# Performance work log

Measured on AMD Instinct MI355X. Metric: run time of the kernel, lower is better.

The kernel has to match this reference:

```python
import jax, jax.numpy as jnp
import numpy as np

P = 2          # patch size
DEPTH = 3
NHEAD = 8
DROP_RATIO = 0.15
LN_EPS = 1e-5


def _ln(x, g, b):
    m = jnp.mean(x, axis=-1, keepdims=True)
    v = jnp.mean((x - m) ** 2, axis=-1, keepdims=True)
    return (x - m) * jax.lax.rsqrt(v + LN_EPS) * g + b


def setup_inputs() -> dict:
    key = jax.random.key(0)
    ks = jax.random.split(key, 16)
    B, C, HW, D, L = 4, 3, 96, 256, DEPTH
    N = (HW // P) ** 2
    s = 0.02
    return {
        "x": jax.random.normal(ks[0], (B, C, HW, HW), jnp.float32),
        "patch_w": jax.random.normal(ks[1], (D, C, P, P), jnp.float32) * s,
        "patch_b": jnp.zeros((D,), jnp.float32),
        "pos": jax.random.normal(ks[2], (1, N, D), jnp.float32) * s,
        "imp_w1": jax.random.normal(ks[3], (D, 256), jnp.float32) * s,
        "imp_b1": jnp.zeros((256,), jnp.float32),
        "imp_w2": jax.random.normal(ks[4], (256, 1), jnp.float32) * s,
        "imp_b2": jnp.zeros((1,), jnp.float32),
        "ln1_g": jnp.ones((L, D), jnp.float32),
        "ln1_b": jnp.zeros((L, D), jnp.float32),
        "qkv_w": jax.random.normal(ks[5], (L, D, 3 * D), jnp.float32) * s,
        "qkv_b": jnp.zeros((L, 3 * D), jnp.float32),
        "proj_w": jax.random.normal(ks[6], (L, D, D), jnp.float32) * s,
        "proj_b": jnp.zeros((L, D), jnp.float32),
        "ln2_g": jnp.ones((L, D), jnp.float32),
        "ln2_b": jnp.zeros((L, D), jnp.float32),
        "mlp_w1": jax.random.normal(ks[7], (L, D, 4 * D), jnp.float32) * s,
        "mlp_b1": jnp.zeros((L, 4 * D), jnp.float32),
        "mlp_w2": jax.random.normal(ks[8], (L, 4 * D, D), jnp.float32) * s,
        "mlp_b2": jnp.zeros((L, D), jnp.float32),
        "out_g": jnp.ones((D,), jnp.float32),
        "out_b": jnp.zeros((D,), jnp.float32),
    }


def reference(x, patch_w, patch_b, pos, imp_w1, imp_b1, imp_w2, imp_b2,
              ln1_g, ln1_b, qkv_w, qkv_b, proj_w, proj_b,
              ln2_g, ln2_b, mlp_w1, mlp_b1, mlp_w2, mlp_b2, out_g, out_b):
    B, C, H, W = x.shape
    D = patch_w.shape[0]
    Hc, Wc = H // P, W // P
    # Patch embed: conv(k=stride=P) == blocked einsum  -> (B, N, D)
    xr = x.reshape(B, C, Hc, P, Wc, P)
    tokens = jnp.einsum('bchpwq,dcpq->bhwd', xr, patch_w).reshape(B, Hc * Wc, D) + patch_b
    tokens = tokens + pos
    B, N, _ = tokens.shape

    # Importance scores -> bottom-k keys masked (Eq.8-10)
    h = jax.nn.relu(tokens @ imp_w1 + imp_b1)
    scores = jax.nn.sigmoid((h @ imp_w2 + imp_b2)[..., 0])  # (B, N)
    k = int(DROP_RATIO * N)
    _, idx = jax.lax.top_k(-scores, k)                      # k smallest scores
    md = jnp.zeros((B, N), bool).at[jnp.arange(B)[:, None], idx].set(True)

    dk = D // NHEAD
    scale = 1.0 / np.sqrt(dk)
    for l in range(DEPTH):
        hln = _ln(tokens, ln1_g[l], ln1_b[l])
        qkv = hln @ qkv_w[l] + qkv_b[l]
        q, kk, v = jnp.split(qkv, 3, axis=-1)
        q = q.reshape(B, N, NHEAD, dk).transpose(0, 2, 1, 3)
        kk = kk.reshape(B, N, NHEAD, dk).transpose(0, 2, 1, 3)
        v = v.reshape(B, N, NHEAD, dk).transpose(0, 2, 1, 3)
        logits = jnp.einsum('bhnd,bhmd->bhnm', q, kk) * scale
        logits = jnp.where(md[:, None, None, :], -jnp.inf, logits)
        attn = jax.nn.softmax(logits, axis=-1)
        out = jnp.einsum('bhnm,bhmd->bhnd', attn, v)
        out = out.transpose(0, 2, 1, 3).reshape(B, N, D)
        tokens = tokens + (out @ proj_w[l] + proj_b[l])
        h2 = _ln(tokens, ln2_g[l], ln2_b[l])
        tokens = tokens + (jax.nn.gelu(h2 @ mlp_w1[l] + mlp_b1[l], approximate=False) @ mlp_w2[l] + mlp_b2[l])

    tokens = _ln(tokens, out_g, out_b)
    return tokens.mean(axis=1)  # (B, D)
```

## Files before the change

kernel.cpp:

```cpp
#include <hip/hip_runtime.h>
#include <hip/hip_bf16.h>
#include <math.h>

#define BATCH 4
#define NTOK  2304
#define DIM   256
#define NHEADS 8
#define HCDIM 48
#define KSEL  345
#define NKEEP 1959
#define NKC   1984
#define KT    31
#define KREM  39
#define LN_EPS 1e-5f
#define QSCALE 0.25508688726880056f

typedef unsigned short u16;
typedef __attribute__((ext_vector_type(8))) short bf16x8;
typedef __attribute__((ext_vector_type(4))) float f32x4;

__device__ __forceinline__ u16 f2bf(float x) {
  union { float f; unsigned u; } v; v.f = x;
  return (u16)((v.u + 0x7FFFu + ((v.u >> 16) & 1u)) >> 16);
}

__device__ __forceinline__ void gload_lds16(const u16* g, u16* l) {
  __builtin_amdgcn_global_load_lds((const __attribute__((address_space(1))) void*)g,
                                   (__attribute__((address_space(3))) void*)l, 16, 0, 0);
}

__global__ __launch_bounds__(256) void k_patch_embed(
    const float* __restrict__ x, const float* __restrict__ pw,
    const float* __restrict__ pb, const float* __restrict__ pos,
    float* __restrict__ tokens) {
  int blk = blockIdx.x;
  int b = blk / NTOK, n = blk % NTOK;
  int hc = n / HCDIM, wc = n % HCDIM;
  __shared__ float xs[12];
  int t = threadIdx.x;
  if (t < 12) {
    int c = t >> 2, p = (t >> 1) & 1, q = t & 1;
    xs[t] = x[((b * 3 + c) * 96 + (hc * 2 + p)) * 96 + (wc * 2 + q)];
  }
  __syncthreads();
  float acc = pb[t];
#pragma unroll
  for (int i = 0; i < 12; ++i) acc += xs[i] * pw[t * 12 + i];
  tokens[(size_t)(b * NTOK + n) * DIM + t] = acc + pos[n * DIM + t];
}

__global__ __launch_bounds__(256) void k_importance(
    const float* __restrict__ tokens, const float* __restrict__ w1,
    const float* __restrict__ b1, const float* __restrict__ w2,
    const float* __restrict__ b2, float* __restrict__ scores) {
  __shared__ float ts[16 * 256];
  __shared__ float hw[16 * 256];
  int base = blockIdx.x * 16;
  int t = threadIdx.x;
  for (int i = t; i < 16 * 256; i += 256) ts[i] = tokens[(size_t)base * 256 + i];
  __syncthreads();
  float acc[16];
#pragma unroll
  for (int r = 0; r < 16; ++r) acc[r] = b1[t];
  for (int i = 0; i < 256; ++i) {
    float w = w1[i * 256 + t];
#pragma unroll
    for (int r = 0; r < 16; ++r) acc[r] += ts[r * 256 + i] * w;
  }
  float w2v = w2[t];
#pragma unroll
  for (int r = 0; r < 16; ++r) hw[r * 256 + t] = fmaxf(acc[r], 0.f) * w2v;
  __syncthreads();
  if (t < 16) {
    float s = b2[0];
    for (int i = 0; i < 256; ++i) s += hw[t * 256 + i];
    scores[base + t] = 1.f / (1.f + expf(-s));
  }
}

__global__ __launch_bounds__(256) void k_select(const float* __restrict__ scores,
                                                int* __restrict__ cmap,
                                                u16* __restrict__ kvc) {
  int b = blockIdx.x, t = threadIdx.x;
  __shared__ unsigned sb[NTOK];
  __shared__ int cnt;
  __shared__ int pfl[256], pfe[256];
  __shared__ int remS;
  for (int i = t; i < NTOK; i += 256) sb[i] = __float_as_uint(scores[b * NTOK + i]);
  __syncthreads();
  unsigned prefix = 0;
  int r = KSEL;
  for (int bit = 31; bit >= 0; --bit) {
    if (t == 0) cnt = 0;
    __syncthreads();
    unsigned bmask = 1u << bit;
    unsigned hmask = (bit == 31) ? 0u : ~((bmask << 1) - 1u);
    int local = 0;
    for (int i = t; i < NTOK; i += 256)
      if ((sb[i] & hmask) == prefix && !(sb[i] & bmask)) local++;
    if (local) atomicAdd(&cnt, local);
    __syncthreads();
    int c0 = cnt;
    if (r > c0) { r -= c0; prefix |= bmask; }
    __syncthreads();
  }
  unsigned v = prefix;
  int cl = 0, ce = 0;
  int j0 = t * 9;
  for (int j = j0; j < j0 + 9; ++j) { cl += (sb[j] < v); ce += (sb[j] == v); }
  pfl[t] = cl; pfe[t] = ce;
  __syncthreads();
  if (t == 0) {
    int pl = 0, pe = 0;
    for (int i = 0; i < 256; ++i) {
      int a = pfl[i], e = pfe[i];
      pfl[i] = pl; pfe[i] = pe;
      pl += a; pe += e;
    }
    remS = KSEL - pl;
  }
  __syncthreads();
  int pl = pfl[t], pe = pfe[t], rem = remS;
  for (int j = j0; j < j0 + 9; ++j) {
    bool less = sb[j] < v, eq = sb[j] == v;
    bool drop = less || (eq && pe < rem);
    int dropped_before = pl + (pe < rem ? pe : rem);
    cmap[b * NTOK + j] = drop ? -1 : (j - dropped_before);
    pl += less; pe += eq;
  }
  for (int i = t; i < (NKC - NKEEP) * 512; i += 256)
    kvc[((size_t)b * NKC + NKEEP) * 512 + i] = 0;
}

__global__ __launch_bounds__(256) void k_ln4bf(
    const float* __restrict__ in, u16* __restrict__ out,
    const float* __restrict__ g, const float* __restrict__ bta) {
  int w = threadIdx.x >> 6, l = threadIdx.x & 63;
  size_t row = (size_t)blockIdx.x * 4 + w;
  float4 v = *(const float4*)(in + row * DIM + l * 4);
  float s = v.x + v.y + v.z + v.w;
  float ss = v.x * v.x + v.y * v.y + v.z * v.z + v.w * v.w;
#pragma unroll
  for (int o = 1; o < 64; o <<= 1) { s += __shfl_xor(s, o); ss += __shfl_xor(ss, o); }
  float m = s * (1.f / DIM);
  float inv = rsqrtf(ss * (1.f / DIM) - m * m + LN_EPS);
  float4 gv = *(const float4*)(g + l * 4);
  float4 bv = *(const float4*)(bta + l * 4);
  union { ushort4 u4; __hip_bfloat162 h2[2]; } o4;
  o4.h2[0] = __float22bfloat162_rn(make_float2((v.x - m) * inv * gv.x + bv.x,
                                               (v.y - m) * inv * gv.y + bv.y));
  o4.h2[1] = __float22bfloat162_rn(make_float2((v.z - m) * inv * gv.z + bv.z,
                                               (v.w - m) * inv * gv.w + bv.w));
  *(ushort4*)(out + row * DIM + l * 4) = o4.u4;
}

__global__ __launch_bounds__(256) void k_lnmean(
    const float* __restrict__ in, const float* __restrict__ g,
    const float* __restrict__ bta, float* __restrict__ part) {
  int chunk = blockIdx.x, b = blockIdx.y;
  int w = threadIdx.x >> 6, l = threadIdx.x & 63;
  float4 gv = *(const float4*)(g + l * 4);
  float4 bv = *(const float4*)(bta + l * 4);
  float4 acc = make_float4(0.f, 0.f, 0.f, 0.f);
  for (int i = 0; i < 16; ++i) {
    size_t row = (size_t)b * NTOK + chunk * 64 + w * 16 + i;
    float4 v = *(const float4*)(in + row * DIM + l * 4);
    float s = v.x + v.y + v.z + v.w;
    float ss = v.x * v.x + v.y * v.y + v.z * v.z + v.w * v.w;
#pragma unroll
    for (int o = 1; o < 64; o <<= 1) { s += __shfl_xor(s, o); ss += __shfl_xor(ss, o); }
    float m = s * (1.f / DIM);
    float inv = rsqrtf(ss * (1.f / DIM) - m * m + LN_EPS);
    acc.x += (v.x - m) * inv * gv.x + bv.x;
    acc.y += (v.y - m) * inv * gv.y + bv.y;
    acc.z += (v.z - m) * inv * gv.z + bv.z;
    acc.w += (v.w - m) * inv * gv.w + bv.w;
  }
  __shared__ float4 red[4][64];
  red[w][l] = acc;
  __syncthreads();
  if (w == 0) {
    float4 a0 = red[0][l], a1 = red[1][l], a2 = red[2][l], a3 = red[3][l];
    float4 tot = make_float4(a0.x + a1.x + a2.x + a3.x, a0.y + a1.y + a2.y + a3.y,
                             a0.z + a1.z + a2.z + a3.z, a0.w + a1.w + a2.w + a3.w);
    *(float4*)(part + ((size_t)b * 36 + chunk) * DIM + l * 4) = tot;
  }
}

__global__ __launch_bounds__(256) void k_mean_final(const float* __restrict__ part,
                                                    float* __restrict__ out) {
  int b = blockIdx.x, d = threadIdx.x;
  float s = 0.f;
  for (int c = 0; c < 36; ++c) s += part[(size_t)(b * 36 + c) * DIM + d];
  out[b * DIM + d] = s * (1.0f / NTOK);
}

__global__ __launch_bounds__(256) void k_wtrans_all(
    const float* __restrict__ qkv_w, const float* __restrict__ proj_w,
    const float* __restrict__ mlp_w1, const float* __restrict__ mlp_w2,
    u16* __restrict__ wq, u16* __restrict__ wp,
    u16* __restrict__ w1, u16* __restrict__ w2) {
  int id = blockIdx.x;
  const float* W; u16* WT; int K, N, m;
  if (id < 576)       { m = id;        K = 256;  N = 768;  W = qkv_w;  WT = wq; }
  else if (id < 768)  { m = id - 576;  K = 256;  N = 256;  W = proj_w; WT = wp; }
  else if (id < 1536) { m = id - 768;  K = 256;  N = 1024; W = mlp_w1; WT = w1; }
  else                { m = id - 1536; K = 1024; N = 256;  W = mlp_w2; WT = w2; }
  int ntiles = N / 32, tilesPerLayer = ntiles * (K / 32);
  int layer = m / tilesPerLayer, tid = m % tilesPerLayer;
  int nb = (tid % ntiles) * 32, kb = (tid / ntiles) * 32;
  const float* Wl = W + (size_t)layer * K * N;
  u16* WTl = WT + (size_t)layer * K * N;
  __shared__ float tile[32][33];
  int tx = threadIdx.x & 31, ty = threadIdx.x >> 5;
  for (int i = 0; i < 32; i += 8) tile[ty + i][tx] = Wl[(size_t)(kb + ty + i) * N + nb + tx];
  __syncthreads();
  for (int i = 0; i < 32; i += 8)
    WTl[(size_t)(nb + ty + i) * K + kb + tx] = f2bf(tile[tx][ty + i]);
}

__global__ __launch_bounds__(256) void k_gemm_bf16(
    const u16* __restrict__ A, const u16* __restrict__ BT,
    const float* __restrict__ bias, u16* __restrict__ outb,
    int K, int N, int act) {
  __shared__ __align__(16) u16 As[2][128 * 32];
  __shared__ __align__(16) u16 Bs[2][128 * 32];
  int t = threadIdx.x;
  int m0 = blockIdx.y * 128, n0 = blockIdx.x * 128;
  int w = t >> 6, l = t & 63, lr = l & 15, qd = l >> 4;
  int wm = (w >> 1) * 64, wn = (w & 1) * 64;
  int sc = ((t & 3) ^ ((t >> 4) & 3)) * 8;
  int rc = (qd ^ ((lr >> 2) & 3)) * 8;
  const u16* gA = A + (size_t)(m0 + w * 16 + (l >> 2)) * K + sc;
  const u16* gA2 = gA + (size_t)64 * K;
  const u16* gB = BT + (size_t)(n0 + w * 16 + (l >> 2)) * K + sc;
  const u16* gB2 = gB + (size_t)64 * K;
  f32x4 acc[4][4];
#pragma unroll
  for (int i = 0; i < 4; ++i)
#pragma unroll
    for (int j = 0; j < 4; ++j)
#pragma unroll
      for (int r = 0; r < 4; ++r) acc[i][j][r] = 0.f;
  gload_lds16(gA, As[0] + w * 512);
  gload_lds16(gA2, As[0] + 2048 + w * 512);
  gload_lds16(gB, Bs[0] + w * 512);
  gload_lds16(gB2, Bs[0] + 2048 + w * 512);
  int nchunks = K >> 5;
  for (int c = 0; c < nchunks; ++c) {
    int buf = c & 1;
    __syncthreads();
    if (c + 1 < nchunks) {
      int k0 = (c + 1) << 5;
      gload_lds16(gA + k0, As[buf ^ 1] + w * 512);
      gload_lds16(gA2 + k0, As[buf ^ 1] + 2048 + w * 512);
      gload_lds16(gB + k0, Bs[buf ^ 1] + w * 512);
      gload_lds16(gB2 + k0, Bs[buf ^ 1] + 2048 + w * 512);
    }
    bf16x8 af[4], bfr[4];
#pragma unroll
    for (int mt = 0; mt < 4; ++mt)
      af[mt] = *(const bf16x8*)(As[buf] + (wm + mt * 16 + lr) * 32 + rc);
#pragma unroll
    for (int nt = 0; nt < 4; ++nt)
      bfr[nt] = *(const bf16x8*)(Bs[buf] + (wn + nt * 16 + lr) * 32 + rc);
#pragma unroll
    for (int mt = 0; mt < 4; ++mt)
#pragma unroll
      for (int nt = 0; nt < 4; ++nt)
        acc[mt][nt] = __builtin_amdgcn_mfma_f32_16x16x32_bf16(af[mt], bfr[nt],
                                                              acc[mt][nt], 0, 0, 0);
  }
#pragma unroll
  for (int mt = 0; mt < 4; ++mt) {
#pragma unroll
    for (int nt = 0; nt < 4; ++nt) {
#pragma unroll
      for (int r = 0; r < 4; ++r) {
        size_t m = (size_t)m0 + wm + mt * 16 + qd * 4 + r;
        int c = n0 + wn + nt * 16 + lr;
        float val = acc[mt][nt][r] + bias[c];
        if (act) val = 0.5f * val * (1.f + erff(val * 0.70710678118654752f));
        outb[m * N + c] = f2bf(val);
      }
    }
  }
}

__global__ __launch_bounds__(256) void k_gemm_qkv(
    const u16* __restrict__ A, const u16* __restrict__ BT,
    const float* __restrict__ bias, const int* __restrict__ cmap,
    u16* __restrict__ Qb, u16* __restrict__ KVc) {
  const int K = 256, N = 768;
  __shared__ __align__(16) u16 As[2][128 * 32];
  __shared__ __align__(16) u16 Bs[2][128 * 32];
  int t = threadIdx.x;
  int m0 = blockIdx.y * 128, n0 = blockIdx.x * 128;
  int w = t >> 6, l = t & 63, lr = l & 15, qd = l >> 4;
  int wm = (w >> 1) * 64, wn = (w & 1) * 64;
  int sc = ((t & 3) ^ ((t >> 4) & 3)) * 8;
  int rc = (qd ^ ((lr >> 2) & 3)) * 8;
  const u16* gA = A + (size_t)(m0 + w * 16 + (l >> 2)) * K + sc;
  const u16* gA2 = gA + (size_t)64 * K;
  const u16* gB = BT + (size_t)(n0 + w * 16 + (l >> 2)) * K + sc;
  const u16* gB2 = gB + (size_t)64 * K;
  f32x4 acc[4][4];
#pragma unroll
  for (int i = 0; i < 4; ++i)
#pragma unroll
    for (int j = 0; j < 4; ++j)
#pragma unroll
      for (int r = 0; r < 4; ++r) acc[i][j][r] = 0.f;
  gload_lds16(gA, As[0] + w * 512);
  gload_lds16(gA2, As[0] + 2048 + w * 512);
  gload_lds16(gB, Bs[0] + w * 512);
  gload_lds16(gB2, Bs[0] + 2048 + w * 512);
  for (int c = 0; c < 8; ++c) {
    int buf = c & 1;
    __syncthreads();
    if (c + 1 < 8) {
      int k0 = (c + 1) << 5;
      gload_lds16(gA + k0, As[buf ^ 1] + w * 512);
      gload_lds16(gA2 + k0, As[buf ^ 1] + 2048 + w * 512);
      gload_lds16(gB + k0, Bs[buf ^ 1] + w * 512);
      gload_lds16(gB2 + k0, Bs[buf ^ 1] + 2048 + w * 512);
    }
    bf16x8 af[4], bfr[4];
#pragma unroll
    for (int mt = 0; mt < 4; ++mt)
      af[mt] = *(const bf16x8*)(As[buf] + (wm + mt * 16 + lr) * 32 + rc);
#pragma unroll
    for (int nt = 0; nt < 4; ++nt)
      bfr[nt] = *(const bf16x8*)(Bs[buf] + (wn + nt * 16 + lr) * 32 + rc);
#pragma unroll
    for (int mt = 0; mt < 4; ++mt)
#pragma unroll
      for (int nt = 0; nt < 4; ++nt)
        acc[mt][nt] = __builtin_amdgcn_mfma_f32_16x16x32_bf16(af[mt], bfr[nt],
                                                              acc[mt][nt], 0, 0, 0);
  }
  bool isQ = (n0 + wn) < 256;
#pragma unroll
  for (int mt = 0; mt < 4; ++mt) {
#pragma unroll
    for (int r = 0; r < 4; ++r) {
      int m = m0 + wm + mt * 16 + qd * 4 + r;
      int cpos = isQ ? 0 : cmap[m];
      int b = m / NTOK;
#pragma unroll
      for (int nt = 0; nt < 4; ++nt) {
        int c = n0 + wn + nt * 16 + lr;
        float val = acc[mt][nt][r] + bias[c];
        if (isQ) {
          Qb[(size_t)m * 256 + c] = f2bf(val * QSCALE);
        } else if (cpos >= 0) {
          KVc[((size_t)b * NKC + cpos) * 512 + (c - 256)] = f2bf(val);
        }
      }
    }
  }
}

__global__ __launch_bounds__(256) void k_gemm_n64(
    const u16* __restrict__ A, const u16* __restrict__ BT,
    const float* __restrict__ bias, const float* __restrict__ res,
    float* __restrict__ outf, int K, int N) {
  __shared__ __align__(16) u16 As[2][64 * 32];
  __shared__ __align__(16) u16 Bs[2][64 * 32];
  int t = threadIdx.x;
  int m0 = blockIdx.y * 64, n0 = blockIdx.x * 64;
  int w = t >> 6, l = t & 63, lr = l & 15, qd = l >> 4;
  int wm = (w >> 1) * 32, wn = (w & 1) * 32;
  int sc = ((t & 3) ^ ((t >> 4) & 3)) * 8;
  int rc = (qd ^ ((lr >> 2) & 3)) * 8;
  const u16* gA = A + (size_t)(m0 + w * 16 + (l >> 2)) * K + sc;
  const u16* gB = BT + (size_t)(n0 + w * 16 + (l >> 2)) * K + sc;
  f32x4 acc[2][2];
#pragma unroll
  for (int i = 0; i < 2; ++i)
#pragma unroll
    for (int j = 0; j < 2; ++j)
#pragma unroll
      for (int r = 0; r < 4; ++r) acc[i][j][r] = 0.f;
  gload_lds16(gA, As[0] + w * 512);
  gload_lds16(gB, Bs[0] + w * 512);
  int nchunks = K >> 5;
  for (int c = 0; c < nchunks; ++c) {
    int buf = c & 1;
    __syncthreads();
    if (c + 1 < nchunks) {
      int k0 = (c + 1) << 5;
      gload_lds16(gA + k0, As[buf ^ 1] + w * 512);
      gload_lds16(gB + k0, Bs[buf ^ 1] + w * 512);
    }
    bf16x8 af[2], bfr[2];
#pragma unroll
    for (int mt = 0; mt < 2; ++mt)
      af[mt] = *(const bf16x8*)(As[buf] + (wm + mt * 16 + lr) * 32 + rc);
#pragma unroll
    for (int nt = 0; nt < 2; ++nt)
      bfr[nt] = *(const bf16x8*)(Bs[buf] + (wn + nt * 16 + lr) * 32 + rc);
#pragma unroll
    for (int mt = 0; mt < 2; ++mt)
#pragma unroll
      for (int nt = 0; nt < 2; ++nt)
        acc[mt][nt] = __builtin_amdgcn_mfma_f32_16x16x32_bf16(af[mt], bfr[nt],
                                                              acc[mt][nt], 0, 0, 0);
  }
#pragma unroll
  for (int mt = 0; mt < 2; ++mt) {
#pragma unroll
    for (int nt = 0; nt < 2; ++nt) {
#pragma unroll
      for (int r = 0; r < 4; ++r) {
        size_t m = (size_t)m0 + wm + mt * 16 + qd * 4 + r;
        int c = n0 + wn + nt * 16 + lr;
        outf[m * N + c] = acc[mt][nt][r] + bias[c] + res[m * N + c];
      }
    }
  }
}

__global__ __launch_bounds__(256) void k_attn6(
    const u16* __restrict__ Qb, const u16* __restrict__ KVc,
    u16* __restrict__ outb) {
  int qt = blockIdx.x, h = blockIdx.y, b = blockIdx.z;
  int t = threadIdx.x, w = t >> 6, l = t & 63, lr = l & 15, qd = l >> 4;
  __shared__ __align__(16) u16 Ks[2][64 * 32];
  __shared__ __align__(16) u16 Vt[2][32][72];
  __shared__ __align__(16) u16 Pq[4][16][72];
  const short ONE = (short)0x3F80;
  int q0 = qt * 64 + w * 16;
  bf16x8 qf = *(const bf16x8*)(Qb + ((size_t)(b * NTOK) + q0 + lr) * 256 + h * 32 + qd * 8);
  const u16* kvb = KVc + (size_t)b * NKC * 512;
  const u16* gK = kvb + (size_t)(t >> 2) * 512 + h * 32 + ((t & 3) ^ ((t >> 4) & 3)) * 8;
  const u16* gV = kvb + (size_t)l * 512 + 256 + h * 32 + w * 8;
  int rc = (qd ^ ((lr >> 2) & 3)) * 8;
  gload_lds16(gK, &Ks[0][w * 512]);
  bf16x8 vr = *(const bf16x8*)(gV);
  f32x4 oa[2];
  f32x4 lacc;
#pragma unroll
  for (int r = 0; r < 4; ++r) { oa[0][r] = 0.f; oa[1][r] = 0.f; lacc[r] = 0.f; }
  bf16x8 ones;
#pragma unroll
  for (int j = 0; j < 8; ++j) ones[j] = ONE;
  for (int kt = 0; kt < KT; ++kt) {
    int buf = kt & 1;
#pragma unroll
    for (int j = 0; j < 8; ++j) Vt[buf][w * 8 + j][l] = (u16)vr[j];
    __syncthreads();
    if (kt + 1 < KT) {
      size_t off = (size_t)(kt + 1) * 64 * 512;
      gload_lds16(gK + off, &Ks[buf ^ 1][w * 512]);
      vr = *(const bf16x8*)(gV + off);
    }
    f32x4 p4[4];
#pragma unroll
    for (int nt = 0; nt < 4; ++nt) {
      bf16x8 kf = *(const bf16x8*)(&Ks[buf][(nt * 16 + lr) * 32 + rc]);
      f32x4 z; z[0] = 0.f; z[1] = 0.f; z[2] = 0.f; z[3] = 0.f;
      p4[nt] = __builtin_amdgcn_mfma_f32_16x16x32_bf16(kf, qf, z, 0, 0, 0);
    }
#pragma unroll
    for (int nt = 0; nt < 4; ++nt)
#pragma unroll
      for (int r = 0; r < 4; ++r) p4[nt][r] = __builtin_amdgcn_exp2f(p4[nt][r]);
#pragma unroll
    for (int nt = 0; nt < 4; ++nt) {
      union { ushort4 u4; __hip_bfloat162 h2[2]; } pu;
      pu.h2[0] = __float22bfloat162_rn(make_float2(p4[nt][0], p4[nt][1]));
      pu.h2[1] = __float22bfloat162_rn(make_float2(p4[nt][2], p4[nt][3]));
      *(ushort4*)(&Pq[w][lr][nt * 16 + qd * 4]) = pu.u4;
    }
    bf16x8 of1 = ones;
    if (kt == KT - 1) {
#pragma unroll
      for (int j = 0; j < 8; ++j) of1[j] = (32 + qd * 8 + j < KREM) ? ONE : (short)0;
    }
#pragma unroll
    for (int kh = 0; kh < 2; ++kh) {
      bf16x8 pf = *(const bf16x8*)(&Pq[w][lr][kh * 32 + qd * 8]);
#pragma unroll
      for (int dh = 0; dh < 2; ++dh) {
        bf16x8 vf = *(const bf16x8*)(&Vt[buf][dh * 16 + lr][kh * 32 + qd * 8]);
        oa[dh] = __builtin_amdgcn_mfma_f32_16x16x32_bf16(pf, vf, oa[dh], 0, 0, 0);
      }
      lacc = __builtin_amdgcn_mfma_f32_16x16x32_bf16(pf, kh ? of1 : ones, lacc, 0, 0, 0);
    }
  }
#pragma unroll
  for (int r = 0; r < 4; ++r) {
    float inv = 1.f / lacc[r];
    size_t row = (size_t)b * NTOK + q0 + qd * 4 + r;
    outb[row * 256 + h * 32 + lr] = f2bf(oa[0][r] * inv);
    outb[row * 256 + h * 32 + 16 + lr] = f2bf(oa[1][r] * inv);
  }
}

extern "C" void kernel_launch(void* const* d_in, const int* in_sizes, int n_in,
                              void* d_out, int out_size, void* d_ws, size_t ws_size,
                              hipStream_t stream) {
  (void)in_sizes; (void)n_in; (void)out_size;
  const float* x       = (const float*)d_in[0];
  const float* patch_w = (const float*)d_in[1];
  const float* patch_b = (const float*)d_in[2];
  const float* pos     = (const float*)d_in[3];
  const float* imp_w1  = (const float*)d_in[4];
  const float* imp_b1  = (const float*)d_in[5];
  const float* imp_w2  = (const float*)d_in[6];
  const float* imp_b2  = (const float*)d_in[7];
  const float* ln1_g   = (const float*)d_in[8];
  const float* ln1_b   = (const float*)d_in[9];
  const float* qkv_w   = (const float*)d_in[10];
  const float* qkv_b   = (const float*)d_in[11];
  const float* proj_w  = (const float*)d_in[12];
  const float* proj_b  = (const float*)d_in[13];
  const float* ln2_g   = (const float*)d_in[14];
  const float* ln2_b   = (const float*)d_in[15];
  const float* mlp_w1  = (const float*)d_in[16];
  const float* mlp_b1  = (const float*)d_in[17];
  const float* mlp_w2  = (const float*)d_in[18];
  const float* mlp_b2  = (const float*)d_in[19];
  const float* out_g   = (const float*)d_in[20];
  const float* out_b   = (const float*)d_in[21];
  float* out = (float*)d_out;

  const int M = BATCH * NTOK;
  const size_t TOK = (size_t)M * DIM;

  char* p = (char*)d_ws;
  float* tokens = (float*)p;       p += TOK * 4;
  float* scoresp = (float*)p;      p += (size_t)M * 4;
  int* cmap = (int*)p;             p += (size_t)M * 4;
  u16* act_bf = (u16*)p;           p += TOK * 2;
  u16* Qb = (u16*)p;               p += TOK * 2;
  u16* kvc = (u16*)p;              p += (size_t)BATCH * NKC * 512 * 2;
  u16* big_bf = (u16*)p;           p += (size_t)M * 1024 * 2;
  u16* wq_t = (u16*)p;             p += (size_t)3 * 768 * 256 * 2;
  u16* wp_t = (u16*)p;             p += (size_t)3 * 256 * 256 * 2;
  u16* w1_t = (u16*)p;             p += (size_t)3 * 1024 * 256 * 2;
  u16* w2_t = (u16*)p;             p += (size_t)3 * 256 * 1024 * 2;
  float* partials = (float*)act_bf;
  if (ws_size < (size_t)(p - (char*)d_ws)) return;

  k_wtrans_all<<<dim3(2304), 256, 0, stream>>>(qkv_w, proj_w, mlp_w1, mlp_w2,
                                               wq_t, wp_t, w1_t, w2_t);
  k_patch_embed<<<dim3(M), 256, 0, stream>>>(x, patch_w, patch_b, pos, tokens);
  k_importance<<<dim3(M / 16), 256, 0, stream>>>(tokens, imp_w1, imp_b1, imp_w2, imp_b2, scoresp);
  k_select<<<dim3(BATCH), 256, 0, stream>>>(scoresp, cmap, kvc);

  for (int l = 0; l < 3; ++l) {
    k_ln4bf<<<dim3(M / 4), 256, 0, stream>>>(tokens, act_bf, ln1_g + l * DIM, ln1_b + l * DIM);
    k_gemm_qkv<<<dim3(6, 72), 256, 0, stream>>>(
        act_bf, wq_t + (size_t)l * 768 * 256, qkv_b + l * 768, cmap, Qb, kvc);
    k_attn6<<<dim3(36, NHEADS, BATCH), 256, 0, stream>>>(Qb, kvc, act_bf);
    k_gemm_n64<<<dim3(4, 144), 256, 0, stream>>>(
        act_bf, wp_t + (size_t)l * 256 * 256, proj_b + l * DIM, tokens, tokens, 256, 256);
    k_ln4bf<<<dim3(M / 4), 256, 0, stream>>>(tokens, act_bf, ln2_g + l * DIM, ln2_b + l * DIM);
    k_gemm_bf16<<<dim3(8, 72), 256, 0, stream>>>(
        act_bf, w1_t + (size_t)l * 1024 * 256, mlp_b1 + l * 1024, big_bf, 256, 1024, 1);
    k_gemm_n64<<<dim3(4, 144), 256, 0, stream>>>(
        big_bf, w2_t + (size_t)l * 256 * 1024, mlp_b2 + l * DIM, tokens, tokens, 1024, 256);
  }
  k_lnmean<<<dim3(36, BATCH), 256, 0, stream>>>(tokens, out_g, out_b, partials);
  k_mean_final<<<dim3(BATCH), 256, 0, stream>>>(partials, out);
}
```

Baseline: 571.3 us.

## Store V transposed from QKV GEMM and load attention V fragments directly

The QKV GEMM epilogue now writes K and V to separate buffers, with V stored transposed (per head-dim row, keys contiguous). The attention kernel then loads its MFMA V operands straight from global memory into registers with prefetching, dropping the per-tile LDS transpose of V and its shared buffer. The cost is scattered 2-byte transposed stores in the GEMM epilogue, which coalesce poorly, plus extra registers for the prefetched fragments.

```diff
diff --git a/kernel.cpp b/kernel.cpp
--- a/kernel.cpp
+++ b/kernel.cpp
@@ -80,7 +80,8 @@
 
 __global__ __launch_bounds__(256) void k_select(const float* __restrict__ scores,
                                                 int* __restrict__ cmap,
-                                                u16* __restrict__ kvc) {
+                                                u16* __restrict__ Kc,
+                                                u16* __restrict__ VT) {
   int b = blockIdx.x, t = threadIdx.x;
   __shared__ unsigned sb[NTOK];
   __shared__ int cnt;
@@ -128,8 +129,12 @@
     cmap[b * NTOK + j] = drop ? -1 : (j - dropped_before);
     pl += less; pe += eq;
   }
-  for (int i = t; i < (NKC - NKEEP) * 512; i += 256)
-    kvc[((size_t)b * NKC + NKEEP) * 512 + i] = 0;
+  for (int i = t; i < (NKC - NKEEP) * 256; i += 256)
+    Kc[((size_t)b * NKC + NKEEP) * 256 + i] = 0;
+  for (int i = t; i < 256 * (NKC - NKEEP); i += 256) {
+    int row = i / (NKC - NKEEP), key = i % (NKC - NKEEP);
+    VT[((size_t)b * 256 + row) * NKC + NKEEP + key] = 0;
+  }
 }
 
 __global__ __launch_bounds__(256) void k_ln4bf(
@@ -290,7 +295,7 @@
 __global__ __launch_bounds__(256) void k_gemm_qkv(
     const u16* __restrict__ A, const u16* __restrict__ BT,
     const float* __restrict__ bias, const int* __restrict__ cmap,
-    u16* __restrict__ Qb, u16* __restrict__ KVc) {
+    u16* __restrict__ Qb, u16* __restrict__ Kc, u16* __restrict__ VT) {
   const int K = 256, N = 768;
   __shared__ __align__(16) u16 As[2][128 * 32];
   __shared__ __align__(16) u16 Bs[2][128 * 32];
@@ -339,22 +344,26 @@
         acc[mt][nt] = __builtin_amdgcn_mfma_f32_16x16x32_bf16(af[mt], bfr[nt],
                                                               acc[mt][nt], 0, 0, 0);
   }
-  bool isQ = (n0 + wn) < 256;
+  int sec = (n0 + wn) >> 8;
 #pragma unroll
   for (int mt = 0; mt < 4; ++mt) {
 #pragma unroll
     for (int r = 0; r < 4; ++r) {
       int m = m0 + wm + mt * 16 + qd * 4 + r;
-      int cpos = isQ ? 0 : cmap[m];
+      int cpos = (sec == 0) ? 0 : cmap[m];
       int b = m / NTOK;
 #pragma unroll
       for (int nt = 0; nt < 4; ++nt) {
         int c = n0 + wn + nt * 16 + lr;
         float val = acc[mt][nt][r] + bias[c];
-        if (isQ) {
+        if (sec == 0) {
           Qb[(size_t)m * 256 + c] = f2bf(val * QSCALE);
         } else if (cpos >= 0) {
-          KVc[((size_t)b * NKC + cpos) * 512 + (c - 256)] = f2bf(val);
+          if (sec == 1) {
+            Kc[((size_t)b * NKC + cpos) * 256 + (c - 256)] = f2bf(val);
+          } else {
+            VT[((size_t)b * 256 + (c - 512)) * NKC + cpos] = f2bf(val);
+          }
         }
       }
     }
@@ -421,23 +430,30 @@
   }
 }
 
-__global__ __launch_bounds__(256) void k_attn6(
-    const u16* __restrict__ Qb, const u16* __restrict__ KVc,
-    u16* __restrict__ outb) {
+__global__ __launch_bounds__(256) void k_attn8(
+    const u16* __restrict__ Qb, const u16* __restrict__ Kc,
+    const u16* __restrict__ VT, u16* __restrict__ outb) {
   int qt = blockIdx.x, h = blockIdx.y, b = blockIdx.z;
   int t = threadIdx.x, w = t >> 6, l = t & 63, lr = l & 15, qd = l >> 4;
   __shared__ __align__(16) u16 Ks[2][64 * 32];
-  __shared__ __align__(16) u16 Vt[2][32][72];
   __shared__ __align__(16) u16 Pq[4][16][72];
   const short ONE = (short)0x3F80;
   int q0 = qt * 64 + w * 16;
   bf16x8 qf = *(const bf16x8*)(Qb + ((size_t)(b * NTOK) + q0 + lr) * 256 + h * 32 + qd * 8);
-  const u16* kvb = KVc + (size_t)b * NKC * 512;
-  const u16* gK = kvb + (size_t)(t >> 2) * 512 + h * 32 + ((t & 3) ^ ((t >> 4) & 3)) * 8;
-  const u16* gV = kvb + (size_t)l * 512 + 256 + h * 32 + w * 8;
+  const u16* kcb = Kc + (size_t)b * NKC * 256 + h * 32;
+  const u16* vtb = VT + ((size_t)b * 256 + h * 32) * NKC;
+  const u16* gK = kcb + (size_t)(t >> 2) * 256 + ((t & 3) ^ ((t >> 4) & 3)) * 8;
   int rc = (qd ^ ((lr >> 2) & 3)) * 8;
   gload_lds16(gK, &Ks[0][w * 512]);
-  bf16x8 vr = *(const bf16x8*)(gV);
+  const u16* gV[4];
+#pragma unroll
+  for (int kh = 0; kh < 2; ++kh)
+#pragma unroll
+    for (int dh = 0; dh < 2; ++dh)
+      gV[kh * 2 + dh] = vtb + (size_t)(dh * 16 + lr) * NKC + kh * 32 + qd * 8;
+  bf16x8 vfc[4], vfn[4];
+#pragma unroll
+  for (int i = 0; i < 4; ++i) vfc[i] = *(const bf16x8*)(gV[i]);
   f32x4 oa[2];
   f32x4 lacc;
 #pragma unroll
@@ -447,13 +463,12 @@
   for (int j = 0; j < 8; ++j) ones[j] = ONE;
   for (int kt = 0; kt < KT; ++kt) {
     int buf = kt & 1;
-#pragma unroll
-    for (int j = 0; j < 8; ++j) Vt[buf][w * 8 + j][l] = (u16)vr[j];
     __syncthreads();
     if (kt + 1 < KT) {
-      size_t off = (size_t)(kt + 1) * 64 * 512;
-      gload_lds16(gK + off, &Ks[buf ^ 1][w * 512]);
-      vr = *(const bf16x8*)(gV + off);
+      int kb = (kt + 1) * 64;
+      gload_lds16(gK + (size_t)kb * 256, &Ks[buf ^ 1][w * 512]);
+#pragma unroll
+      for (int i = 0; i < 4; ++i) vfn[i] = *(const bf16x8*)(gV[i] + kb);
     }
     f32x4 p4[4];
 #pragma unroll
@@ -482,11 +497,14 @@
     for (int kh = 0; kh < 2; ++kh) {
       bf16x8 pf = *(const bf16x8*)(&Pq[w][lr][kh * 32 + qd * 8]);
 #pragma unroll
-      for (int dh = 0; dh < 2; ++dh) {
-        bf16x8 vf = *(const bf16x8*)(&Vt[buf][dh * 16 + lr][kh * 32 + qd * 8]);
-        oa[dh] = __builtin_amdgcn_mfma_f32_16x16x32_bf16(pf, vf, oa[dh], 0, 0, 0);
-      }
+      for (int dh = 0; dh < 2; ++dh)
+        oa[dh] = __builtin_amdgcn_mfma_f32_16x16x32_bf16(pf, vfc[kh * 2 + dh],
+                                                         oa[dh], 0, 0, 0);
       lacc = __builtin_amdgcn_mfma_f32_16x16x32_bf16(pf, kh ? of1 : ones, lacc, 0, 0, 0);
+    }
+    if (kt + 1 < KT) {
+#pragma unroll
+      for (int i = 0; i < 4; ++i) vfc[i] = vfn[i];
     }
   }
 #pragma unroll
@@ -535,7 +553,8 @@
   int* cmap = (int*)p;             p += (size_t)M * 4;
   u16* act_bf = (u16*)p;           p += TOK * 2;
   u16* Qb = (u16*)p;               p += TOK * 2;
-  u16* kvc = (u16*)p;              p += (size_t)BATCH * NKC * 512 * 2;
+  u16* kc = (u16*)p;               p += (size_t)BATCH * NKC * 256 * 2;
+  u16* vt = (u16*)p;               p += (size_t)BATCH * 256 * NKC * 2;
   u16* big_bf = (u16*)p;           p += (size_t)M * 1024 * 2;
   u16* wq_t = (u16*)p;             p += (size_t)3 * 768 * 256 * 2;
   u16* wp_t = (u16*)p;             p += (size_t)3 * 256 * 256 * 2;
@@ -548,13 +567,13 @@
                                                wq_t, wp_t, w1_t, w2_t);
   k_patch_embed<<<dim3(M), 256, 0, stream>>>(x, patch_w, patch_b, pos, tokens);
   k_importance<<<dim3(M / 16), 256, 0, stream>>>(tokens, imp_w1, imp_b1, imp_w2, imp_b2, scoresp);
-  k_select<<<dim3(BATCH), 256, 0, stream>>>(scoresp, cmap, kvc);
+  k_select<<<dim3(BATCH), 256, 0, stream>>>(scoresp, cmap, kc, vt);
 
   for (int l = 0; l < 3; ++l) {
     k_ln4bf<<<dim3(M / 4), 256, 0, stream>>>(tokens, act_bf, ln1_g + l * DIM, ln1_b + l * DIM);
     k_gemm_qkv<<<dim3(6, 72), 256, 0, stream>>>(
-        act_bf, wq_t + (size_t)l * 768 * 256, qkv_b + l * 768, cmap, Qb, kvc);
-    k_attn6<<<dim3(36, NHEADS, BATCH), 256, 0, stream>>>(Qb, kvc, act_bf);
+        act_bf, wq_t + (size_t)l * 768 * 256, qkv_b + l * 768, cmap, Qb, kc, vt);
+    k_attn8<<<dim3(36, NHEADS, BATCH), 256, 0, stream>>>(Qb, kc, vt, act_bf);
     k_gemm_n64<<<dim3(4, 144), 256, 0, stream>>>(
         act_bf, wp_t + (size_t)l * 256 * 256, proj_b + l * DIM, tokens, tokens, 256, 256);
     k_ln4bf<<<dim3(M / 4), 256, 0, stream>>>(tokens, act_bf, ln2_g + l * DIM, ln2_b + l * DIM);
```

Measured after the change: 670.3 us. 17.3% more time.

## Fold LayerNorm into GEMM epilogues via row statistics and precomputed weight vectors

Applied to the files above, without the earlier changes.

Removes the standalone LayerNorm kernels. The residual GEMMs now also write a bf16 copy of the tokens and atomically accumulate per-row sum and sum-of-squares. The LN gamma is folded into the transposed weights, and the mean and beta terms are applied in the QKV and MLP1 epilogues using precomputed u and v vectors. This saves six launches and one read/write pass over the tokens per LN, at the cost of float atomics and variance computed from raw unnormalized bf16 inputs, which may lose precision.

```diff
diff --git a/kernel.cpp b/kernel.cpp
--- a/kernel.cpp
+++ b/kernel.cpp
@@ -32,11 +32,12 @@
 __global__ __launch_bounds__(256) void k_patch_embed(
     const float* __restrict__ x, const float* __restrict__ pw,
     const float* __restrict__ pb, const float* __restrict__ pos,
-    float* __restrict__ tokens) {
+    float* __restrict__ tokens, u16* __restrict__ tokb, float* __restrict__ rs0) {
   int blk = blockIdx.x;
   int b = blk / NTOK, n = blk % NTOK;
   int hc = n / HCDIM, wc = n % HCDIM;
   __shared__ float xs[12];
+  __shared__ float ps[4], pss[4];
   int t = threadIdx.x;
   if (t < 12) {
     int c = t >> 2, p = (t >> 1) & 1, q = t & 1;
@@ -46,7 +47,20 @@
   float acc = pb[t];
 #pragma unroll
   for (int i = 0; i < 12; ++i) acc += xs[i] * pw[t * 12 + i];
-  tokens[(size_t)(b * NTOK + n) * DIM + t] = acc + pos[n * DIM + t];
+  float val = acc + pos[n * DIM + t];
+  size_t row = (size_t)(b * NTOK + n);
+  tokens[row * DIM + t] = val;
+  tokb[row * DIM + t] = f2bf(val);
+  float s = val, ss = val * val;
+#pragma unroll
+  for (int o = 1; o < 64; o <<= 1) { s += __shfl_xor(s, o); ss += __shfl_xor(ss, o); }
+  int wv = t >> 6, ln = t & 63;
+  if (ln == 0) { ps[wv] = s; pss[wv] = ss; }
+  __syncthreads();
+  if (t == 0) {
+    rs0[2 * row] = ps[0] + ps[1] + ps[2] + ps[3];
+    rs0[2 * row + 1] = pss[0] + pss[1] + pss[2] + pss[3];
+  }
 }
 
 __global__ __launch_bounds__(256) void k_importance(
@@ -132,28 +146,6 @@
     kvc[((size_t)b * NKC + NKEEP) * 512 + i] = 0;
 }
 
-__global__ __launch_bounds__(256) void k_ln4bf(
-    const float* __restrict__ in, u16* __restrict__ out,
-    const float* __restrict__ g, const float* __restrict__ bta) {
-  int w = threadIdx.x >> 6, l = threadIdx.x & 63;
-  size_t row = (size_t)blockIdx.x * 4 + w;
-  float4 v = *(const float4*)(in + row * DIM + l * 4);
-  float s = v.x + v.y + v.z + v.w;
-  float ss = v.x * v.x + v.y * v.y + v.z * v.z + v.w * v.w;
-#pragma unroll
-  for (int o = 1; o < 64; o <<= 1) { s += __shfl_xor(s, o); ss += __shfl_xor(ss, o); }
-  float m = s * (1.f / DIM);
-  float inv = rsqrtf(ss * (1.f / DIM) - m * m + LN_EPS);
-  float4 gv = *(const float4*)(g + l * 4);
-  float4 bv = *(const float4*)(bta + l * 4);
-  union { ushort4 u4; __hip_bfloat162 h2[2]; } o4;
-  o4.h2[0] = __float22bfloat162_rn(make_float2((v.x - m) * inv * gv.x + bv.x,
-                                               (v.y - m) * inv * gv.y + bv.y));
-  o4.h2[1] = __float22bfloat162_rn(make_float2((v.z - m) * inv * gv.z + bv.z,
-                                               (v.w - m) * inv * gv.w + bv.w));
-  *(ushort4*)(out + row * DIM + l * 4) = o4.u4;
-}
-
 __global__ __launch_bounds__(256) void k_lnmean(
     const float* __restrict__ in, const float* __restrict__ g,
     const float* __restrict__ bta, float* __restrict__ part) {
@@ -198,14 +190,15 @@
 __global__ __launch_bounds__(256) void k_wtrans_all(
     const float* __restrict__ qkv_w, const float* __restrict__ proj_w,
     const float* __restrict__ mlp_w1, const float* __restrict__ mlp_w2,
+    const float* __restrict__ g1, const float* __restrict__ g2,
     u16* __restrict__ wq, u16* __restrict__ wp,
     u16* __restrict__ w1, u16* __restrict__ w2) {
   int id = blockIdx.x;
-  const float* W; u16* WT; int K, N, m;
-  if (id < 576)       { m = id;        K = 256;  N = 768;  W = qkv_w;  WT = wq; }
-  else if (id < 768)  { m = id - 576;  K = 256;  N = 256;  W = proj_w; WT = wp; }
-  else if (id < 1536) { m = id - 768;  K = 256;  N = 1024; W = mlp_w1; WT = w1; }
-  else                { m = id - 1536; K = 1024; N = 256;  W = mlp_w2; WT = w2; }
+  const float* W; const float* gs; u16* WT; int K, N, m;
+  if (id < 576)       { m = id;        K = 256;  N = 768;  W = qkv_w;  WT = wq; gs = g1; }
+  else if (id < 768)  { m = id - 576;  K = 256;  N = 256;  W = proj_w; WT = wp; gs = nullptr; }
+  else if (id < 1536) { m = id - 768;  K = 256;  N = 1024; W = mlp_w1; WT = w1; gs = g2; }
+  else                { m = id - 1536; K = 1024; N = 256;  W = mlp_w2; WT = w2; gs = nullptr; }
   int ntiles = N / 32, tilesPerLayer = ntiles * (K / 32);
   int layer = m / tilesPerLayer, tid = m % tilesPerLayer;
   int nb = (tid % ntiles) * 32, kb = (tid / ntiles) * 32;
@@ -215,14 +208,48 @@
   int tx = threadIdx.x & 31, ty = threadIdx.x >> 5;
   for (int i = 0; i < 32; i += 8) tile[ty + i][tx] = Wl[(size_t)(kb + ty + i) * N + nb + tx];
   __syncthreads();
+  float gsc = gs ? gs[layer * 256 + kb + tx] : 1.f;
   for (int i = 0; i < 32; i += 8)
-    WTl[(size_t)(nb + ty + i) * K + kb + tx] = f2bf(tile[tx][ty + i]);
-}
-
-__global__ __launch_bounds__(256) void k_gemm_bf16(
+    WTl[(size_t)(nb + ty + i) * K + kb + tx] = f2bf(tile[tx][ty + i] * gsc);
+}
+
+__global__ __launch_bounds__(256) void k_uv(
+    const float* __restrict__ qkv_w, const float* __restrict__ g1,
+    const float* __restrict__ b1, const float* __restrict__ mlp_w1,
+    const float* __restrict__ g2, const float* __restrict__ b2,
+    float* __restrict__ uq, float* __restrict__ vq,
+    float* __restrict__ u1, float* __restrict__ v1) {
+  int id = blockIdx.x * 256 + threadIdx.x;
+  if (blockIdx.x < 9) {
+    int l = id / 768, n = id % 768;
+    const float* W = qkv_w + (size_t)l * 256 * 768;
+    const float* g = g1 + l * 256; const float* bb = b1 + l * 256;
+    float u = 0.f, v = 0.f;
+    for (int k = 0; k < 256; ++k) {
+      float wv = W[(size_t)k * 768 + n];
+      u += bb[k] * wv; v += g[k] * wv;
+    }
+    uq[id] = u; vq[id] = v;
+  } else {
+    int id2 = id - 9 * 256;
+    int l = id2 / 1024, n = id2 % 1024;
+    const float* W = mlp_w1 + (size_t)l * 256 * 1024;
+    const float* g = g2 + l * 256; const float* bb = b2 + l * 256;
+    float u = 0.f, v = 0.f;
+    for (int k = 0; k < 256; ++k) {
+      float wv = W[(size_t)k * 1024 + n];
+      u += bb[k] * wv; v += g[k] * wv;
+    }
+    u1[id2] = u; v1[id2] = v;
+  }
+}
+
+__global__ __launch_bounds__(256) void k_gemm_mlp1(
     const u16* __restrict__ A, const u16* __restrict__ BT,
-    const float* __restrict__ bias, u16* __restrict__ outb,
-    int K, int N, int act) {
+    const float* __restrict__ bias, const float* __restrict__ rs,
+    const float* __restrict__ uvec, const float* __restrict__ vvec,
+    u16* __restrict__ outb) {
+  const int K = 256, N = 1024;
   __shared__ __align__(16) u16 As[2][128 * 32];
   __shared__ __align__(16) u16 Bs[2][128 * 32];
   int t = threadIdx.x;
@@ -246,11 +273,10 @@
   gload_lds16(gA2, As[0] + 2048 + w * 512);
   gload_lds16(gB, Bs[0] + w * 512);
   gload_lds16(gB2, Bs[0] + 2048 + w * 512);
-  int nchunks = K >> 5;
-  for (int c = 0; c < nchunks; ++c) {
+  for (int c = 0; c < 8; ++c) {
     int buf = c & 1;
     __syncthreads();
-    if (c + 1 < nchunks) {
+    if (c + 1 < 8) {
       int k0 = (c + 1) << 5;
       gload_lds16(gA + k0, As[buf ^ 1] + w * 512);
       gload_lds16(gA2 + k0, As[buf ^ 1] + 2048 + w * 512);
@@ -271,16 +297,26 @@
         acc[mt][nt] = __builtin_amdgcn_mfma_f32_16x16x32_bf16(af[mt], bfr[nt],
                                                               acc[mt][nt], 0, 0, 0);
   }
+  float bb[4], uu[4], vv[4];
+#pragma unroll
+  for (int nt = 0; nt < 4; ++nt) {
+    int c = n0 + wn + nt * 16 + lr;
+    bb[nt] = bias[c]; uu[nt] = uvec[c]; vv[nt] = vvec[c];
+  }
 #pragma unroll
   for (int mt = 0; mt < 4; ++mt) {
 #pragma unroll
-    for (int nt = 0; nt < 4; ++nt) {
-#pragma unroll
-      for (int r = 0; r < 4; ++r) {
-        size_t m = (size_t)m0 + wm + mt * 16 + qd * 4 + r;
+    for (int r = 0; r < 4; ++r) {
+      size_t m = (size_t)m0 + wm + mt * 16 + qd * 4 + r;
+      float s0 = rs[2 * m], s1 = rs[2 * m + 1];
+      float mean = s0 * (1.f / 256);
+      float inv = rsqrtf(s1 * (1.f / 256) - mean * mean + LN_EPS);
+      float fm = mean * inv;
+#pragma unroll
+      for (int nt = 0; nt < 4; ++nt) {
         int c = n0 + wn + nt * 16 + lr;
-        float val = acc[mt][nt][r] + bias[c];
-        if (act) val = 0.5f * val * (1.f + erff(val * 0.70710678118654752f));
+        float val = inv * acc[mt][nt][r] + bb[nt] + uu[nt] - fm * vv[nt];
+        val = 0.5f * val * (1.f + erff(val * 0.70710678118654752f));
         outb[m * N + c] = f2bf(val);
       }
     }
@@ -290,6 +326,8 @@
 __global__ __launch_bounds__(256) void k_gemm_qkv(
     const u16* __restrict__ A, const u16* __restrict__ BT,
     const float* __restrict__ bias, const int* __restrict__ cmap,
+    const float* __restrict__ rs, const float* __restrict__ uvec,
+    const float* __restrict__ vvec,
     u16* __restrict__ Qb, u16* __restrict__ KVc) {
   const int K = 256, N = 768;
   __shared__ __align__(16) u16 As[2][128 * 32];
@@ -340,17 +378,27 @@
                                                               acc[mt][nt], 0, 0, 0);
   }
   bool isQ = (n0 + wn) < 256;
+  float bb[4], uu[4], vv[4];
+#pragma unroll
+  for (int nt = 0; nt < 4; ++nt) {
+    int c = n0 + wn + nt * 16 + lr;
+    bb[nt] = bias[c]; uu[nt] = uvec[c]; vv[nt] = vvec[c];
+  }
 #pragma unroll
   for (int mt = 0; mt < 4; ++mt) {
 #pragma unroll
     for (int r = 0; r < 4; ++r) {
       int m = m0 + wm + mt * 16 + qd * 4 + r;
+      float s0 = rs[2 * (size_t)m], s1 = rs[2 * (size_t)m + 1];
+      float mean = s0 * (1.f / 256);
+      float inv = rsqrtf(s1 * (1.f / 256) - mean * mean + LN_EPS);
+      float fm = mean * inv;
       int cpos = isQ ? 0 : cmap[m];
       int b = m / NTOK;
 #pragma unroll
       for (int nt = 0; nt < 4; ++nt) {
         int c = n0 + wn + nt * 16 + lr;
-        float val = acc[mt][nt][r] + bias[c];
+        float val = inv * acc[mt][nt][r] + bb[nt] + uu[nt] - fm * vv[nt];
         if (isQ) {
           Qb[(size_t)m * 256 + c] = f2bf(val * QSCALE);
         } else if (cpos >= 0) {
@@ -361,10 +409,12 @@
   }
 }
 
-__global__ __launch_bounds__(256) void k_gemm_n64(
+__global__ __launch_bounds__(256) void k_gemm_n64s(
     const u16* __restrict__ A, const u16* __restrict__ BT,
     const float* __restrict__ bias, const float* __restrict__ res,
-    float* __restrict__ outf, int K, int N) {
+    float* __restrict__ outf, u16* __restrict__ outb, float* __restrict__ rsOut,
+    int K) {
+  const int N = 256;
   __shared__ __align__(16) u16 As[2][64 * 32];
   __shared__ __align__(16) u16 Bs[2][64 * 32];
   int t = threadIdx.x;
@@ -410,12 +460,22 @@
 #pragma unroll
   for (int mt = 0; mt < 2; ++mt) {
 #pragma unroll
-    for (int nt = 0; nt < 2; ++nt) {
-#pragma unroll
-      for (int r = 0; r < 4; ++r) {
-        size_t m = (size_t)m0 + wm + mt * 16 + qd * 4 + r;
+    for (int r = 0; r < 4; ++r) {
+      size_t m = (size_t)m0 + wm + mt * 16 + qd * 4 + r;
+      float s = 0.f, ss = 0.f;
+#pragma unroll
+      for (int nt = 0; nt < 2; ++nt) {
         int c = n0 + wn + nt * 16 + lr;
-        outf[m * N + c] = acc[mt][nt][r] + bias[c] + res[m * N + c];
+        float val = acc[mt][nt][r] + bias[c] + res[m * N + c];
+        outf[m * N + c] = val;
+        outb[m * N + c] = f2bf(val);
+        s += val; ss += val * val;
+      }
+#pragma unroll
+      for (int o = 1; o < 16; o <<= 1) { s += __shfl_xor(s, o); ss += __shfl_xor(ss, o); }
+      if (lr == 0) {
+        atomicAdd(&rsOut[2 * m], s);
+        atomicAdd(&rsOut[2 * m + 1], ss);
       }
     }
   }
@@ -534,6 +594,7 @@
   float* scoresp = (float*)p;      p += (size_t)M * 4;
   int* cmap = (int*)p;             p += (size_t)M * 4;
   u16* act_bf = (u16*)p;           p += TOK * 2;
+  u16* tok_bf = (u16*)p;           p += TOK * 2;
   u16* Qb = (u16*)p;               p += TOK * 2;
   u16* kvc = (u16*)p;              p += (size_t)BATCH * NKC * 512 * 2;
   u16* big_bf = (u16*)p;           p += (size_t)M * 1024 * 2;
@@ -541,27 +602,41 @@
   u16* wp_t = (u16*)p;             p += (size_t)3 * 256 * 256 * 2;
   u16* w1_t = (u16*)p;             p += (size_t)3 * 1024 * 256 * 2;
   u16* w2_t = (u16*)p;             p += (size_t)3 * 256 * 1024 * 2;
+  float* uq = (float*)p;           p += (size_t)3 * 768 * 4;
+  float* vq = (float*)p;           p += (size_t)3 * 768 * 4;
+  float* u1 = (float*)p;           p += (size_t)3 * 1024 * 4;
+  float* v1 = (float*)p;           p += (size_t)3 * 1024 * 4;
+  float* rowstat = (float*)p;      p += (size_t)7 * M * 2 * 4;
   float* partials = (float*)act_bf;
   if (ws_size < (size_t)(p - (char*)d_ws)) return;
 
+  hipMemsetAsync(rowstat, 0, (size_t)7 * M * 2 * 4, stream);
   k_wtrans_all<<<dim3(2304), 256, 0, stream>>>(qkv_w, proj_w, mlp_w1, mlp_w2,
-                                               wq_t, wp_t, w1_t, w2_t);
-  k_patch_embed<<<dim3(M), 256, 0, stream>>>(x, patch_w, patch_b, pos, tokens);
+                                               ln1_g, ln2_g, wq_t, wp_t, w1_t, w2_t);
+  k_uv<<<dim3(21), 256, 0, stream>>>(qkv_w, ln1_g, ln1_b, mlp_w1, ln2_g, ln2_b,
+                                     uq, vq, u1, v1);
+  k_patch_embed<<<dim3(M), 256, 0, stream>>>(x, patch_w, patch_b, pos,
+                                             tokens, tok_bf, rowstat);
   k_importance<<<dim3(M / 16), 256, 0, stream>>>(tokens, imp_w1, imp_b1, imp_w2, imp_b2, scoresp);
   k_select<<<dim3(BATCH), 256, 0, stream>>>(scoresp, cmap, kvc);
 
   for (int l = 0; l < 3; ++l) {
-    k_ln4bf<<<dim3(M / 4), 256, 0, stream>>>(tokens, act_bf, ln1_g + l * DIM, ln1_b + l * DIM);
+    float* rs_in  = rowstat + (size_t)(2 * l) * M * 2;
+    float* rs_mid = rowstat + (size_t)(2 * l + 1) * M * 2;
+    float* rs_out = rowstat + (size_t)(2 * l + 2) * M * 2;
     k_gemm_qkv<<<dim3(6, 72), 256, 0, stream>>>(
-        act_bf, wq_t + (size_t)l * 768 * 256, qkv_b + l * 768, cmap, Qb, kvc);
+        tok_bf, wq_t + (size_t)l * 768 * 256, qkv_b + l * 768, cmap,
+        rs_in, uq + l * 768, vq + l * 768, Qb, kvc);
     k_attn6<<<dim3(36, NHEADS, BATCH), 256, 0, stream>>>(Qb, kvc, act_bf);
-    k_gemm_n64<<<dim3(4, 144), 256, 0, stream>>>(
-        act_bf, wp_t + (size_t)l * 256 * 256, proj_b + l * DIM, tokens, tokens, 256, 256);
-    k_ln4bf<<<dim3(M / 4), 256, 0, stream>>>(tokens, act_bf, ln2_g + l * DIM, ln2_b + l * DIM);
-    k_gemm_bf16<<<dim3(8, 72), 256, 0, stream>>>(
-        act_bf, w1_t + (size_t)l * 1024 * 256, mlp_b1 + l * 1024, big_bf, 256, 1024, 1);
-    k_gemm_n64<<<dim3(4, 144), 256, 0, stream>>>(
-        big_bf, w2_t + (size_t)l * 256 * 1024, mlp_b2 + l * DIM, tokens, tokens, 1024, 256);
+    k_gemm_n64s<<<dim3(4, 144), 256, 0, stream>>>(
+        act_bf, wp_t + (size_t)l * 256 * 256, proj_b + l * DIM, tokens,
+        tokens, tok_bf, rs_mid, 256);
+    k_gemm_mlp1<<<dim3(8, 72), 256, 0, stream>>>(
+        tok_bf, w1_t + (size_t)l * 1024 * 256, mlp_b1 + l * 1024,
+        rs_mid, u1 + l * 1024, v1 + l * 1024, big_bf);
+    k_gemm_n64s<<<dim3(4, 144), 256, 0, stream>>>(
+        big_bf, w2_t + (size_t)l * 256 * 1024, mlp_b2 + l * DIM, tokens,
+        tokens, tok_bf, rs_out, 1024);
   }
   k_lnmean<<<dim3(36, BATCH), 256, 0, stream>>>(tokens, out_g, out_b, partials);
   k_mean_final<<<dim3(BATCH), 256, 0, stream>>>(partials, out);
```

New measurement: 610.1 us. +6.8%, slower.

## Split attention KV range across two blocks and combine partial outputs

Applied to the files above, without the earlier changes.

Attention is split over the key dimension into two halves, each handled by a separate block that writes unnormalized fp32 output and row-sum partials. A new combine kernel sums the halves, normalizes, and writes the bf16 output. This doubles the block count to improve occupancy and tail balance across CUs. The cost is extra global memory traffic for the fp32 partials and an extra launch per layer.

```diff
diff --git a/kernel.cpp b/kernel.cpp
--- a/kernel.cpp
+++ b/kernel.cpp
@@ -421,10 +421,13 @@
   }
 }
 
-__global__ __launch_bounds__(256) void k_attn6(
+__global__ __launch_bounds__(256) void k_attn6s(
     const u16* __restrict__ Qb, const u16* __restrict__ KVc,
-    u16* __restrict__ outb) {
-  int qt = blockIdx.x, h = blockIdx.y, b = blockIdx.z;
+    float* __restrict__ Opart, float* __restrict__ lpart) {
+  int qt = blockIdx.x, h = blockIdx.y;
+  int b = blockIdx.z >> 1, half = blockIdx.z & 1;
+  int t0 = half * 16;
+  int ntiles = half ? (KT - 16) : 16;
   int t = threadIdx.x, w = t >> 6, l = t & 63, lr = l & 15, qd = l >> 4;
   __shared__ __align__(16) u16 Ks[2][64 * 32];
   __shared__ __align__(16) u16 Vt[2][32][72];
@@ -432,7 +435,7 @@
   const short ONE = (short)0x3F80;
   int q0 = qt * 64 + w * 16;
   bf16x8 qf = *(const bf16x8*)(Qb + ((size_t)(b * NTOK) + q0 + lr) * 256 + h * 32 + qd * 8);
-  const u16* kvb = KVc + (size_t)b * NKC * 512;
+  const u16* kvb = KVc + (size_t)b * NKC * 512 + (size_t)t0 * 64 * 512;
   const u16* gK = kvb + (size_t)(t >> 2) * 512 + h * 32 + ((t & 3) ^ ((t >> 4) & 3)) * 8;
   const u16* gV = kvb + (size_t)l * 512 + 256 + h * 32 + w * 8;
   int rc = (qd ^ ((lr >> 2) & 3)) * 8;
@@ -445,12 +448,12 @@
   bf16x8 ones;
 #pragma unroll
   for (int j = 0; j < 8; ++j) ones[j] = ONE;
-  for (int kt = 0; kt < KT; ++kt) {
+  for (int kt = 0; kt < ntiles; ++kt) {
     int buf = kt & 1;
 #pragma unroll
     for (int j = 0; j < 8; ++j) Vt[buf][w * 8 + j][l] = (u16)vr[j];
     __syncthreads();
-    if (kt + 1 < KT) {
+    if (kt + 1 < ntiles) {
       size_t off = (size_t)(kt + 1) * 64 * 512;
       gload_lds16(gK + off, &Ks[buf ^ 1][w * 512]);
       vr = *(const bf16x8*)(gV + off);
@@ -474,7 +477,7 @@
       *(ushort4*)(&Pq[w][lr][nt * 16 + qd * 4]) = pu.u4;
     }
     bf16x8 of1 = ones;
-    if (kt == KT - 1) {
+    if (t0 + kt == KT - 1) {
 #pragma unroll
       for (int j = 0; j < 8; ++j) of1[j] = (32 + qd * 8 + j < KREM) ? ONE : (short)0;
     }
@@ -489,13 +492,31 @@
       lacc = __builtin_amdgcn_mfma_f32_16x16x32_bf16(pf, kh ? of1 : ones, lacc, 0, 0, 0);
     }
   }
+  const int M = BATCH * NTOK;
 #pragma unroll
   for (int r = 0; r < 4; ++r) {
-    float inv = 1.f / lacc[r];
-    size_t row = (size_t)b * NTOK + q0 + qd * 4 + r;
-    outb[row * 256 + h * 32 + lr] = f2bf(oa[0][r] * inv);
-    outb[row * 256 + h * 32 + 16 + lr] = f2bf(oa[1][r] * inv);
-  }
+    size_t grow = (size_t)b * NTOK + q0 + qd * 4 + r;
+    size_t orow = (size_t)half * M + grow;
+    Opart[orow * 256 + h * 32 + lr] = oa[0][r];
+    Opart[orow * 256 + h * 32 + 16 + lr] = oa[1][r];
+    if (lr == 0) lpart[orow * 8 + h] = lacc[r];
+  }
+}
+
+__global__ __launch_bounds__(256) void k_attn_comb(
+    const float* __restrict__ Opart, const float* __restrict__ lpart,
+    u16* __restrict__ outb) {
+  const int M = BATCH * NTOK;
+  int w = threadIdx.x >> 6, l = threadIdx.x & 63;
+  size_t grow = (size_t)blockIdx.x * 4 + w;
+  int h = l >> 3;
+  float4 o0 = *(const float4*)(Opart + grow * 256 + l * 4);
+  float4 o1 = *(const float4*)(Opart + ((size_t)M + grow) * 256 + l * 4);
+  float inv = 1.f / (lpart[grow * 8 + h] + lpart[((size_t)M + grow) * 8 + h]);
+  union { ushort4 u4; __hip_bfloat162 h2[2]; } o4;
+  o4.h2[0] = __float22bfloat162_rn(make_float2((o0.x + o1.x) * inv, (o0.y + o1.y) * inv));
+  o4.h2[1] = __float22bfloat162_rn(make_float2((o0.z + o1.z) * inv, (o0.w + o1.w) * inv));
+  *(ushort4*)(outb + grow * 256 + l * 4) = o4.u4;
 }
 
 extern "C" void kernel_launch(void* const* d_in, const int* in_sizes, int n_in,
@@ -541,6 +562,8 @@
   u16* wp_t = (u16*)p;             p += (size_t)3 * 256 * 256 * 2;
   u16* w1_t = (u16*)p;             p += (size_t)3 * 1024 * 256 * 2;
   u16* w2_t = (u16*)p;             p += (size_t)3 * 256 * 1024 * 2;
+  float* Opart = (float*)p;        p += (size_t)2 * TOK * 4;
+  float* lpart = (float*)p;        p += (size_t)2 * M * 8 * 4;
   float* partials = (float*)act_bf;
   if (ws_size < (size_t)(p - (char*)d_ws)) return;
 
@@ -554,7 +577,8 @@
     k_ln4bf<<<dim3(M / 4), 256, 0, stream>>>(tokens, act_bf, ln1_g + l * DIM, ln1_b + l * DIM);
     k_gemm_qkv<<<dim3(6, 72), 256, 0, stream>>>(
         act_bf, wq_t + (size_t)l * 768 * 256, qkv_b + l * 768, cmap, Qb, kvc);
-    k_attn6<<<dim3(36, NHEADS, BATCH), 256, 0, stream>>>(Qb, kvc, act_bf);
+    k_attn6s<<<dim3(36, NHEADS, BATCH * 2), 256, 0, stream>>>(Qb, kvc, Opart, lpart);
+    k_attn_comb<<<dim3(M / 4), 256, 0, stream>>>(Opart, lpart, act_bf);
     k_gemm_n64<<<dim3(4, 144), 256, 0, stream>>>(
         act_bf, wp_t + (size_t)l * 256 * 256, proj_b + l * DIM, tokens, tokens, 256, 256);
     k_ln4bf<<<dim3(M / 4), 256, 0, stream>>>(tokens, act_bf, ln2_g + l * DIM, ln2_b + l * DIM);
```

Measured after the change: 573.6 us. Within noise of the previous version (+0.4%).
